# Optimization experiments

Measured on AMD Instinct MI355X. Metric: run time of the kernel, lower is better.

The kernel has to match this reference:

```python
import jax, jax.numpy as jnp
import numpy as np

D_MODEL = 1024
N_HEADS = 16
D_K = D_MODEL // N_HEADS
EPS = 1e-8


def _l2_rownorm(x):
    # RowNormActivation: normalize each row (last dim) to unit L2 norm
    return x * jax.lax.rsqrt(jnp.sum(x * x, axis=-1, keepdims=True) + EPS)


def setup_inputs() -> dict:
    key = jax.random.key(0)
    ks = jax.random.split(key, 11)
    B, S = 2, 2048
    sc = 1.0 / np.sqrt(D_MODEL)
    inp = {
        "Q": jax.random.normal(ks[0], (B, S, D_MODEL), jnp.float32),
        "K": jax.random.normal(ks[1], (B, S, D_MODEL), jnp.float32),
        "V": jax.random.normal(ks[2], (B, S, D_MODEL), jnp.float32),
        "Wq_w": jax.random.normal(ks[3], (D_MODEL, D_MODEL), jnp.float32) * sc,
        "Wq_b": jnp.zeros((D_MODEL,), jnp.float32),
        "Wk_w": jax.random.normal(ks[4], (D_MODEL, D_MODEL), jnp.float32) * sc,
        "Wk_b": jnp.zeros((D_MODEL,), jnp.float32),
        "Wv_w": jax.random.normal(ks[5], (D_MODEL, D_MODEL), jnp.float32) * sc,
        "Wv_b": jnp.zeros((D_MODEL,), jnp.float32),
        "Wo_w": jax.random.normal(ks[6], (D_MODEL, D_MODEL), jnp.float32) * sc,
        "Wo_b": jnp.zeros((D_MODEL,), jnp.float32),
    }
    return inp


def reference(Q, K, V, Wq_w, Wq_b, Wk_w, Wk_b, Wv_w, Wv_b, Wo_w, Wo_b):
    B, S, _ = Q.shape
    # torch Linear: y = x @ W.T + b
    q = (Q @ Wq_w.T + Wq_b).reshape(B, S, N_HEADS, D_K).transpose(0, 2, 1, 3)
    k = (K @ Wk_w.T + Wk_b).reshape(B, S, N_HEADS, D_K).transpose(0, 2, 1, 3)
    v = (V @ Wv_w.T + Wv_b).reshape(B, S, N_HEADS, D_K).transpose(0, 2, 1, 3)
    qn = _l2_rownorm(q)
    kn = _l2_rownorm(k)
    scores = jnp.einsum("bhqd,bhkd->bhqk", qn, kn)
    attn = scores * scores  # squared similarity, no softmax (dropout=0 / eval)
    out = jnp.einsum("bhqk,bhkd->bhqd", attn, v)
    out = out.transpose(0, 2, 1, 3).reshape(B, S, D_MODEL)
    return out @ Wo_w.T + Wo_b
```

## Files before the change

### kernel.cpp

```cpp
#include <hip/hip_runtime.h>
#include <hip/hip_bf16.h>


#define D_MODEL 1024
#define N_HEADS 16
#define D_K     64
#define BATCH   2
#define SEQ     2048
#define M_TOT   (BATCH * SEQ)

typedef short  s16x8 __attribute__((ext_vector_type(8)));
typedef float  f32x4 __attribute__((ext_vector_type(4)));
typedef unsigned short ushort_t;
typedef ushort_t us4 __attribute__((ext_vector_type(4)));

__device__ __forceinline__ ushort_t f2bf(float f) {
    union { float f; unsigned int u; } x; x.f = f;
    unsigned int u = x.u;
    return (ushort_t)((u + 0x7fffu + ((u >> 16) & 1u)) >> 16);
}
__device__ __forceinline__ float bf2f(ushort_t h) {
    union { unsigned int u; float f; } x; x.u = ((unsigned int)h) << 16;
    return x.f;
}
__device__ __forceinline__ unsigned int pack2bf(float a, float b) {
    union { __hip_bfloat162 h; unsigned int u; } x;
    x.h = __float22bfloat162_rn(float2{a, b});
    return x.u;
}

__device__ __forceinline__ void gload_lds16(const ushort_t* g, ushort_t* l) {
    __builtin_amdgcn_global_load_lds(
        (__attribute__((address_space(1))) void*)(ushort_t*)g,
        (__attribute__((address_space(3))) void*)l, 16, 0, 0);
}

#define WAIT_VM(n)  asm volatile("s_waitcnt vmcnt(" #n ")" ::: "memory")
#define WAIT_LGKM0  asm volatile("s_waitcnt lgkmcnt(0)" ::: "memory")
#define BARRIER     asm volatile("s_barrier" ::: "memory")

struct ConvArgs {
    const float* src[11];
    ushort_t*    dst[11];
    int          n[11];
};

__global__ __launch_bounds__(256) void convert_kernel(ConvArgs a) {
    const int t = blockIdx.y;
    const int i = (blockIdx.x * 256 + threadIdx.x) * 4;
    if (i >= a.n[t]) return;
    const float4 v = *(const float4*)(a.src[t] + i);
    us4 p;
    p[0] = f2bf(v.x); p[1] = f2bf(v.y); p[2] = f2bf(v.z); p[3] = f2bf(v.w);
    *(us4*)(a.dst[t] + i) = p;
}

template <int BM, int MODE>
__device__ __forceinline__ void gemm_body(
    ushort_t* __restrict__ smem,
    const ushort_t* __restrict__ A,
    const ushort_t* __restrict__ W,
    const ushort_t* __restrict__ bias,
    ushort_t* __restrict__ out,
    float* __restrict__ outf,
    int bx, int by)
{
    static_assert(BM == 64 || BM == 128, "");
    constexpr int K    = 1024;
    constexpr int MF   = BM / 32;
    constexpr int BUFW = (BM + 128) * 64;
    constexpr int NIT  = K / 64;

    const int t    = threadIdx.x;
    const int wave = t >> 6;
    const int lane = t & 63;
    const int quad = lane >> 4;
    const int lc   = lane & 15;
    const int wm   = wave >> 1;
    const int wn   = wave & 1;
    const int m0   = bx * BM;
    const int n0   = by * 128;

    f32x4 acc[MF][4];
    const f32x4 zero = {0.f, 0.f, 0.f, 0.f};
#pragma unroll
    for (int i = 0; i < MF; ++i)
#pragma unroll
        for (int j = 0; j < 4; ++j) acc[i][j] = zero;

    auto stage = [&](int buf, int k0) {
        ushort_t* Ast = smem + buf * BUFW;
        ushort_t* Bst = Ast + BM * 64;
#pragma unroll
        for (int c = 0; c < MF; ++c) {
            int idx = c * 256 + t;
            int row = idx >> 3, phys = idx & 7;
            int col = (phys ^ (row & 7)) * 8;
            gload_lds16(A + (size_t)(m0 + row) * K + k0 + col, Ast + idx * 8);
        }
#pragma unroll
        for (int c = 0; c < 4; ++c) {
            int idx = c * 256 + t;
            int row = idx >> 3, phys = idx & 7;
            int col = (phys ^ (row & 7)) * 8;
            gload_lds16(W + (size_t)(n0 + row) * K + k0 + col, Bst + idx * 8);
        }
    };
    auto comp = [&](int buf) {
        ushort_t* Ast = smem + buf * BUFW;
        ushort_t* Bst = Ast + BM * 64;
#pragma unroll
        for (int ks = 0; ks < 2; ++ks) {
            const int ph = ((ks * 4 + quad) ^ (lc & 7)) * 8;
            s16x8 a[MF], b[4];
#pragma unroll
            for (int i = 0; i < MF; ++i)
                a[i] = *(const s16x8*)(Ast + (wm * (BM / 2) + i * 16 + lc) * 64 + ph);
#pragma unroll
            for (int i = 0; i < 4; ++i)
                b[i] = *(const s16x8*)(Bst + (wn * 64 + i * 16 + lc) * 64 + ph);
#pragma unroll
            for (int mf = 0; mf < MF; ++mf)
#pragma unroll
                for (int nf = 0; nf < 4; ++nf)
                    acc[mf][nf] = __builtin_amdgcn_mfma_f32_16x16x32_bf16(
                        a[mf], b[nf], acc[mf][nf], 0, 0, 0);
        }
    };

    stage(0, 0);
    stage(1, 64);
    for (int it = 0; it < NIT - 2; ++it) {
        if constexpr (BM == 128) WAIT_VM(8); else WAIT_VM(6);
        BARRIER;
        comp(it & 1);
        WAIT_LGKM0;
        BARRIER;
        stage(it & 1, (it + 2) * 64);
    }
    if constexpr (BM == 128) WAIT_VM(8); else WAIT_VM(6);
    BARRIER;
    comp((NIT - 2) & 1);
    WAIT_VM(0);
    BARRIER;
    comp((NIT - 1) & 1);

    float bv[4];
#pragma unroll
    for (int nf = 0; nf < 4; ++nf) bv[nf] = bf2f(bias[n0 + wn * 64 + nf * 16 + lc]);

    if (MODE == 0) {
#pragma unroll
        for (int mf = 0; mf < MF; ++mf)
#pragma unroll
            for (int nf = 0; nf < 4; ++nf)
#pragma unroll
                for (int r = 0; r < 4; ++r) {
                    int mg = m0 + wm * (BM / 2) + mf * 16 + quad * 4 + r;
                    int ng = n0 + wn * 64 + nf * 16 + lc;
                    outf[(size_t)mg * D_MODEL + ng] = acc[mf][nf][r] + bv[nf];
                }
    } else if (MODE == 1) {
#pragma unroll
        for (int mf = 0; mf < MF; ++mf)
#pragma unroll
            for (int r = 0; r < 4; ++r) {
                float ss = 0.f;
#pragma unroll
                for (int nf = 0; nf < 4; ++nf) {
                    float v = acc[mf][nf][r] + bv[nf];
                    acc[mf][nf][r] = v;
                    ss += v * v;
                }
                ss += __shfl_xor(ss, 1);
                ss += __shfl_xor(ss, 2);
                ss += __shfl_xor(ss, 4);
                ss += __shfl_xor(ss, 8);
                float inv = rsqrtf(ss + 1e-8f);
                int mg = m0 + wm * (BM / 2) + mf * 16 + quad * 4 + r;
                int b  = mg >> 11;
                int s  = mg & 2047;
#pragma unroll
                for (int nf = 0; nf < 4; ++nf) {
                    int ng = n0 + wn * 64 + nf * 16 + lc;
                    int h = ng >> 6, d = ng & 63;
                    out[(((size_t)(b * N_HEADS + h)) * SEQ + s) * D_K + d] =
                        f2bf(acc[mf][nf][r] * inv);
                }
            }
    } else {
        __syncthreads();
        ushort_t* vt = smem + wave * (64 * 72);
#pragma unroll
        for (int mf = 0; mf < 4; ++mf)
#pragma unroll
            for (int nf = 0; nf < 4; ++nf) {
                us4 p;
#pragma unroll
                for (int r = 0; r < 4; ++r) p[r] = f2bf(acc[mf][nf][r] + bv[nf]);
                *(us4*)(vt + (nf * 16 + lc) * 72 + mf * 16 + quad * 4) = p;
            }
        WAIT_LGKM0;
#pragma unroll
        for (int r = 0; r < 8; ++r) {
            int d  = r * 8 + (lane >> 3);
            int so = (lane & 7) * 8;
            uint4 val = *(const uint4*)(vt + d * 72 + so);
            int mg = m0 + wm * 64 + so;
            int b  = mg >> 11;
            int s  = mg & 2047;
            int ng = n0 + wn * 64 + d;
            int h = ng >> 6, dh = ng & 63;
            *(uint4*)(out + (((size_t)(b * N_HEADS + h)) * D_K + dh) * SEQ + s) = val;
        }
    }
}

__global__ __launch_bounds__(256) void qkv_kernel(
    const ushort_t* __restrict__ Qb, const ushort_t* __restrict__ Kb,
    const ushort_t* __restrict__ Vb,
    const ushort_t* __restrict__ Wq, const ushort_t* __restrict__ Wk,
    const ushort_t* __restrict__ Wv,
    const ushort_t* __restrict__ bq, const ushort_t* __restrict__ bk,
    const ushort_t* __restrict__ bv,
    ushort_t* __restrict__ qn, ushort_t* __restrict__ kn,
    ushort_t* __restrict__ vT)
{
    __shared__ __align__(16) ushort_t smem[2 * (128 + 128) * 64];
    const int z = blockIdx.z;
    if (z == 0)
        gemm_body<128, 1>(smem, Qb, Wq, bq, qn, nullptr, blockIdx.x, blockIdx.y);
    else if (z == 1)
        gemm_body<128, 1>(smem, Kb, Wk, bk, kn, nullptr, blockIdx.x, blockIdx.y);
    else
        gemm_body<128, 2>(smem, Vb, Wv, bv, vT, nullptr, blockIdx.x, blockIdx.y);
}

__global__ __launch_bounds__(256) void wo_kernel(
    const ushort_t* __restrict__ A, const ushort_t* __restrict__ W,
    const ushort_t* __restrict__ bias, float* __restrict__ outf)
{
    __shared__ __align__(16) ushort_t smem[2 * (64 + 128) * 64];
    gemm_body<64, 0>(smem, A, W, bias, nullptr, outf, blockIdx.x, blockIdx.y);
}

__global__ __launch_bounds__(256) void attn_kernel(
    const ushort_t* __restrict__ qn,
    const ushort_t* __restrict__ kn,
    const ushort_t* __restrict__ vT,
    ushort_t* __restrict__ attn_out)
{
    __shared__ __align__(16) ushort_t smem[2 * 8192 + 4 * 32 * 72];

    const int t    = threadIdx.x;
    const int wave = t >> 6;
    const int lane = t & 63;
    const int quad = lane >> 4;
    const int lc   = lane & 15;
    const int bh   = blockIdx.x;
    const int qt   = blockIdx.y;
    const int b    = bh >> 4;
    const int h    = bh & 15;

    const ushort_t* qb = qn + (size_t)bh * SEQ * D_K;
    const ushort_t* kb = kn + (size_t)bh * SEQ * D_K;
    const ushort_t* vb = vT + (size_t)bh * D_K * SEQ;
    const int q0 = qt * 128 + wave * 32;

    s16x8 aq[2][2];
#pragma unroll
    for (int mf = 0; mf < 2; ++mf)
#pragma unroll
        for (int ks = 0; ks < 2; ++ks)
            aq[mf][ks] = *(const s16x8*)(qb + (size_t)(q0 + mf * 16 + lc) * D_K +
                                         ks * 32 + quad * 8);

    f32x4 oacc[2][4];
    const f32x4 zero = {0.f, 0.f, 0.f, 0.f};
#pragma unroll
    for (int mf = 0; mf < 2; ++mf)
#pragma unroll
        for (int df = 0; df < 4; ++df) oacc[mf][df] = zero;

    ushort_t* pl = smem + 2 * 8192 + wave * 32 * 72;

    auto stage = [&](int buf, int j0) {
        ushort_t* kst = smem + buf * 8192;
        ushort_t* vst = kst + 4096;
#pragma unroll
        for (int c = 0; c < 2; ++c) {
            int idx = c * 256 + t;
            int row = idx >> 3, phys = idx & 7;
            int col = (phys ^ (row & 7)) * 8;
            gload_lds16(kb + (size_t)(j0 + row) * D_K + col, kst + idx * 8);
            gload_lds16(vb + (size_t)row * SEQ + j0 + col, vst + idx * 8);
        }
    };
    auto comp = [&](int buf) {
        ushort_t* kst = smem + buf * 8192;
        ushort_t* vst = kst + 4096;
        const int ph0 = ((0 * 4 + quad) ^ (lc & 7)) * 8;
        const int ph1 = ((1 * 4 + quad) ^ (lc & 7)) * 8;
        s16x8 bk[4][2];
#pragma unroll
        for (int jf = 0; jf < 4; ++jf) {
            bk[jf][0] = *(const s16x8*)(kst + (jf * 16 + lc) * 64 + ph0);
            bk[jf][1] = *(const s16x8*)(kst + (jf * 16 + lc) * 64 + ph1);
        }
        f32x4 s[4][2];
#pragma unroll
        for (int jf = 0; jf < 4; ++jf)
#pragma unroll
            for (int mf = 0; mf < 2; ++mf) {
                s[jf][mf] = zero;
#pragma unroll
                for (int ks = 0; ks < 2; ++ks)
                    s[jf][mf] = __builtin_amdgcn_mfma_f32_16x16x32_bf16(
                        bk[jf][ks], aq[mf][ks], s[jf][mf], 0, 0, 0);
            }
#pragma unroll
        for (int jf = 0; jf < 4; ++jf)
#pragma unroll
            for (int mf = 0; mf < 2; ++mf) {
                float p0 = s[jf][mf][0] * s[jf][mf][0];
                float p1 = s[jf][mf][1] * s[jf][mf][1];
                float p2 = s[jf][mf][2] * s[jf][mf][2];
                float p3 = s[jf][mf][3] * s[jf][mf][3];
                uint2 w = {pack2bf(p0, p1), pack2bf(p2, p3)};
                *(uint2*)(pl + (mf * 16 + lc) * 72 + jf * 16 + quad * 4) = w;
            }
        s16x8 bvf[4][2];
#pragma unroll
        for (int df = 0; df < 4; ++df) {
            bvf[df][0] = *(const s16x8*)(vst + (df * 16 + lc) * 64 + ph0);
            bvf[df][1] = *(const s16x8*)(vst + (df * 16 + lc) * 64 + ph1);
        }
        WAIT_LGKM0;
        s16x8 aa[2][2];
#pragma unroll
        for (int mf = 0; mf < 2; ++mf)
#pragma unroll
            for (int ks = 0; ks < 2; ++ks)
                aa[mf][ks] = *(const s16x8*)(pl + (mf * 16 + lc) * 72 +
                                             ks * 32 + quad * 8);
#pragma unroll
        for (int mf = 0; mf < 2; ++mf)
#pragma unroll
            for (int df = 0; df < 4; ++df)
#pragma unroll
                for (int ks = 0; ks < 2; ++ks)
                    oacc[mf][df] = __builtin_amdgcn_mfma_f32_16x16x32_bf16(
                        aa[mf][ks], bvf[df][ks], oacc[mf][df], 0, 0, 0);
    };

    constexpr int NT = 32;
    stage(0, 0);
    stage(1, 64);
    for (int it = 0; it < NT - 2; ++it) {
        WAIT_VM(4);
        BARRIER;
        comp(it & 1);
        WAIT_LGKM0;
        BARRIER;
        stage(it & 1, (it + 2) * 64);
    }
    WAIT_VM(4);
    BARRIER;
    comp((NT - 2) & 1);
    WAIT_VM(0);
    BARRIER;
    comp((NT - 1) & 1);

#pragma unroll
    for (int mf = 0; mf < 2; ++mf)
#pragma unroll
        for (int df = 0; df < 4; ++df)
#pragma unroll
            for (int r = 0; r < 4; ++r) {
                int s = q0 + mf * 16 + quad * 4 + r;
                int d = df * 16 + lc;
                attn_out[((size_t)(b * SEQ + s)) * D_MODEL + h * D_K + d] =
                    f2bf(oacc[mf][df][r]);
            }
}

extern "C" void kernel_launch(void* const* d_in, const int* in_sizes, int n_in,
                              void* d_out, int out_size, void* d_ws, size_t ws_size,
                              hipStream_t stream)
{
    const float* Qf   = (const float*)d_in[0];
    const float* Kf   = (const float*)d_in[1];
    const float* Vf   = (const float*)d_in[2];
    const float* Wqf  = (const float*)d_in[3];
    const float* Wqbf = (const float*)d_in[4];
    const float* Wkf  = (const float*)d_in[5];
    const float* Wkbf = (const float*)d_in[6];
    const float* Wvf  = (const float*)d_in[7];
    const float* Wvbf = (const float*)d_in[8];
    const float* Wof  = (const float*)d_in[9];
    const float* Wobf = (const float*)d_in[10];

    const size_t NM = (size_t)M_TOT * D_MODEL;
    const size_t NW = (size_t)D_MODEL * D_MODEL;
    const size_t NB = D_MODEL;

    ushort_t* p = (ushort_t*)d_ws;
    ushort_t* Qb  = p;  p += NM;
    ushort_t* Kb  = p;  p += NM;
    ushort_t* Vb  = p;  p += NM;
    ushort_t* Wq  = p;  p += NW;
    ushort_t* Wk  = p;  p += NW;
    ushort_t* Wv  = p;  p += NW;
    ushort_t* Wo  = p;  p += NW;
    ushort_t* bq  = p;  p += NB;
    ushort_t* bk  = p;  p += NB;
    ushort_t* bvv = p;  p += NB;
    ushort_t* bo  = p;  p += NB;
    ushort_t* qn  = p;  p += NM;
    ushort_t* kn  = p;  p += NM;
    ushort_t* vT  = p;  p += NM;
    ushort_t* ao  = p;  p += NM;

    ConvArgs ca;
    ca.src[0] = Qf;   ca.dst[0] = Qb;  ca.n[0] = (int)NM;
    ca.src[1] = Kf;   ca.dst[1] = Kb;  ca.n[1] = (int)NM;
    ca.src[2] = Vf;   ca.dst[2] = Vb;  ca.n[2] = (int)NM;
    ca.src[3] = Wqf;  ca.dst[3] = Wq;  ca.n[3] = (int)NW;
    ca.src[4] = Wkf;  ca.dst[4] = Wk;  ca.n[4] = (int)NW;
    ca.src[5] = Wvf;  ca.dst[5] = Wv;  ca.n[5] = (int)NW;
    ca.src[6] = Wof;  ca.dst[6] = Wo;  ca.n[6] = (int)NW;
    ca.src[7] = Wqbf; ca.dst[7] = bq;  ca.n[7] = (int)NB;
    ca.src[8] = Wkbf; ca.dst[8] = bk;  ca.n[8] = (int)NB;
    ca.src[9] = Wvbf; ca.dst[9] = bvv; ca.n[9] = (int)NB;
    ca.src[10] = Wobf; ca.dst[10] = bo; ca.n[10] = (int)NB;

    dim3 blk(256);
    convert_kernel<<<dim3((unsigned)(NM / (256 * 4)), 11), blk, 0, stream>>>(ca);

    qkv_kernel<<<dim3(M_TOT / 128, D_MODEL / 128, 3), blk, 0, stream>>>(
        Qb, Kb, Vb, Wq, Wk, Wv, bq, bk, bvv, qn, kn, vT);
    attn_kernel<<<dim3(BATCH * N_HEADS, SEQ / 128), blk, 0, stream>>>(qn, kn, vT, ao);
    wo_kernel<<<dim3(M_TOT / 64, D_MODEL / 128), blk, 0, stream>>>(
        ao, Wo, bo, (float*)d_out);
}
```

Measured before the change: 243.7 us.

## Split attention QK work by key-rows across waves with shared swizzled P tile

The attention kernel now has each wave compute scores for 16 keys against all 128 block queries, holding all Q fragments in registers, and write squared scores into a block-shared XOR-swizzled P tile. After a barrier, each wave reads its 32 query rows of P and runs the PV MFMAs. This removes the per-wave reloading of the whole K tile from LDS and avoids the padded per-wave P buffer. In exchange it adds an extra block barrier per iteration and raises register pressure from holding 16 Q fragments per lane.

```diff
diff --git a/kernel.cpp b/kernel.cpp
--- a/kernel.cpp
+++ b/kernel.cpp
@@ -250,7 +250,8 @@
     const ushort_t* __restrict__ vT,
     ushort_t* __restrict__ attn_out)
 {
-    __shared__ __align__(16) ushort_t smem[2 * 8192 + 4 * 32 * 72];
+    __shared__ __align__(16) ushort_t smem[2 * 8192];
+    __shared__ __align__(16) ushort_t Pl[128 * 64];
 
     const int t    = threadIdx.x;
     const int wave = t >> 6;
@@ -265,14 +266,14 @@
     const ushort_t* qb = qn + (size_t)bh * SEQ * D_K;
     const ushort_t* kb = kn + (size_t)bh * SEQ * D_K;
     const ushort_t* vb = vT + (size_t)bh * D_K * SEQ;
-    const int q0 = qt * 128 + wave * 32;
-
-    s16x8 aq[2][2];
-#pragma unroll
-    for (int mf = 0; mf < 2; ++mf)
+    const int q0 = qt * 128;
+
+    s16x8 qf[8][2];
+#pragma unroll
+    for (int mf = 0; mf < 8; ++mf)
 #pragma unroll
         for (int ks = 0; ks < 2; ++ks)
-            aq[mf][ks] = *(const s16x8*)(qb + (size_t)(q0 + mf * 16 + lc) * D_K +
+            qf[mf][ks] = *(const s16x8*)(qb + (size_t)(q0 + mf * 16 + lc) * D_K +
                                          ks * 32 + quad * 8);
 
     f32x4 oacc[2][4];
@@ -281,8 +282,6 @@
     for (int mf = 0; mf < 2; ++mf)
 #pragma unroll
         for (int df = 0; df < 4; ++df) oacc[mf][df] = zero;
-
-    ushort_t* pl = smem + 2 * 8192 + wave * 32 * 72;
 
     auto stage = [&](int buf, int j0) {
         ushort_t* kst = smem + buf * 8192;
@@ -296,91 +295,91 @@
             gload_lds16(vb + (size_t)row * SEQ + j0 + col, vst + idx * 8);
         }
     };
-    auto comp = [&](int buf) {
+
+    auto qk = [&](int buf) {
         ushort_t* kst = smem + buf * 8192;
-        ushort_t* vst = kst + 4096;
-        const int ph0 = ((0 * 4 + quad) ^ (lc & 7)) * 8;
-        const int ph1 = ((1 * 4 + quad) ^ (lc & 7)) * 8;
-        s16x8 bk[4][2];
-#pragma unroll
-        for (int jf = 0; jf < 4; ++jf) {
-            bk[jf][0] = *(const s16x8*)(kst + (jf * 16 + lc) * 64 + ph0);
-            bk[jf][1] = *(const s16x8*)(kst + (jf * 16 + lc) * 64 + ph1);
-        }
-        f32x4 s[4][2];
-#pragma unroll
-        for (int jf = 0; jf < 4; ++jf)
-#pragma unroll
-            for (int mf = 0; mf < 2; ++mf) {
-                s[jf][mf] = zero;
+        s16x8 ak[2];
+#pragma unroll
+        for (int ks = 0; ks < 2; ++ks)
+            ak[ks] = *(const s16x8*)(kst + (wave * 16 + lc) * 64 +
+                                     (((ks * 4 + quad) ^ (lc & 7)) * 8));
+        const int log8 = wave * 4 + quad;
+#pragma unroll
+        for (int mf = 0; mf < 8; ++mf) {
+            f32x4 st = zero;
+#pragma unroll
+            for (int ks = 0; ks < 2; ++ks)
+                st = __builtin_amdgcn_mfma_f32_16x16x32_bf16(ak[ks], qf[mf][ks], st, 0, 0, 0);
+            uint2 w;
+            w.x = pack2bf(st[0] * st[0], st[1] * st[1]);
+            w.y = pack2bf(st[2] * st[2], st[3] * st[3]);
+            const int row = mf * 16 + lc;
+            *(uint2*)(Pl + row * 64 + (log8 ^ lc) * 4) = w;
+        }
+    };
+
+    auto pv = [&](int buf) {
+        ushort_t* vst = smem + buf * 8192 + 4096;
+        s16x8 bvf[4][2];
+#pragma unroll
+        for (int df = 0; df < 4; ++df)
+#pragma unroll
+            for (int ks = 0; ks < 2; ++ks)
+                bvf[df][ks] = *(const s16x8*)(vst + (df * 16 + lc) * 64 +
+                                              (((ks * 4 + quad) ^ (lc & 7)) * 8));
+        s16x8 aa[2][2];
+#pragma unroll
+        for (int mfp = 0; mfp < 2; ++mfp)
+#pragma unroll
+            for (int ks = 0; ks < 2; ++ks) {
+                const int row = wave * 32 + mfp * 16 + lc;
+                const int l0  = ks * 8 + quad * 2;
+                uint2 lo = *(const uint2*)(Pl + row * 64 + ((l0 ^ lc) * 4));
+                uint2 hi = *(const uint2*)(Pl + row * 64 + (((l0 + 1) ^ lc) * 4));
+                union { unsigned int u[4]; s16x8 v; } m;
+                m.u[0] = lo.x; m.u[1] = lo.y; m.u[2] = hi.x; m.u[3] = hi.y;
+                aa[mfp][ks] = m.v;
+            }
+#pragma unroll
+        for (int mfp = 0; mfp < 2; ++mfp)
+#pragma unroll
+            for (int df = 0; df < 4; ++df)
 #pragma unroll
                 for (int ks = 0; ks < 2; ++ks)
-                    s[jf][mf] = __builtin_amdgcn_mfma_f32_16x16x32_bf16(
-                        bk[jf][ks], aq[mf][ks], s[jf][mf], 0, 0, 0);
-            }
-#pragma unroll
-        for (int jf = 0; jf < 4; ++jf)
-#pragma unroll
-            for (int mf = 0; mf < 2; ++mf) {
-                float p0 = s[jf][mf][0] * s[jf][mf][0];
-                float p1 = s[jf][mf][1] * s[jf][mf][1];
-                float p2 = s[jf][mf][2] * s[jf][mf][2];
-                float p3 = s[jf][mf][3] * s[jf][mf][3];
-                uint2 w = {pack2bf(p0, p1), pack2bf(p2, p3)};
-                *(uint2*)(pl + (mf * 16 + lc) * 72 + jf * 16 + quad * 4) = w;
-            }
-        s16x8 bvf[4][2];
-#pragma unroll
-        for (int df = 0; df < 4; ++df) {
-            bvf[df][0] = *(const s16x8*)(vst + (df * 16 + lc) * 64 + ph0);
-            bvf[df][1] = *(const s16x8*)(vst + (df * 16 + lc) * 64 + ph1);
-        }
-        WAIT_LGKM0;
-        s16x8 aa[2][2];
-#pragma unroll
-        for (int mf = 0; mf < 2; ++mf)
-#pragma unroll
-            for (int ks = 0; ks < 2; ++ks)
-                aa[mf][ks] = *(const s16x8*)(pl + (mf * 16 + lc) * 72 +
-                                             ks * 32 + quad * 8);
-#pragma unroll
-        for (int mf = 0; mf < 2; ++mf)
-#pragma unroll
-            for (int df = 0; df < 4; ++df)
-#pragma unroll
-                for (int ks = 0; ks < 2; ++ks)
-                    oacc[mf][df] = __builtin_amdgcn_mfma_f32_16x16x32_bf16(
-                        aa[mf][ks], bvf[df][ks], oacc[mf][df], 0, 0, 0);
+                    oacc[mfp][df] = __builtin_amdgcn_mfma_f32_16x16x32_bf16(
+                        aa[mfp][ks], bvf[df][ks], oacc[mfp][df], 0, 0, 0);
     };
 
     constexpr int NT = 32;
     stage(0, 0);
     stage(1, 64);
-    for (int it = 0; it < NT - 2; ++it) {
-        WAIT_VM(4);
+    for (int it = 0; it < NT; ++it) {
+        if (it < NT - 1) { WAIT_VM(4); } else { WAIT_VM(0); }
         BARRIER;
-        comp(it & 1);
+        qk(it & 1);
         WAIT_LGKM0;
         BARRIER;
-        stage(it & 1, (it + 2) * 64);
+        pv(it & 1);
+        if (it < NT - 2) {
+            WAIT_LGKM0;
+            BARRIER;
+            stage(it & 1, (it + 2) * 64);
+        } else if (it == NT - 2) {
+            WAIT_LGKM0;
+            BARRIER;
+        }
     }
-    WAIT_VM(4);
-    BARRIER;
-    comp((NT - 2) & 1);
-    WAIT_VM(0);
-    BARRIER;
-    comp((NT - 1) & 1);
-
-#pragma unroll
-    for (int mf = 0; mf < 2; ++mf)
+
+#pragma unroll
+    for (int mfp = 0; mfp < 2; ++mfp)
 #pragma unroll
         for (int df = 0; df < 4; ++df)
 #pragma unroll
             for (int r = 0; r < 4; ++r) {
-                int s = q0 + mf * 16 + quad * 4 + r;
+                int s = q0 + wave * 32 + mfp * 16 + quad * 4 + r;
                 int d = df * 16 + lc;
                 attn_out[((size_t)(b * SEQ + s)) * D_MODEL + h * D_K + d] =
-                    f2bf(oacc[mf][df][r]);
+                    f2bf(oacc[mfp][df][r]);
             }
 }
 
```

New measurement: 226.4 us, median of 2. 1.08x faster.
